# Kernel optimization log

Measured on AMD Instinct MI355X. Metric: run time of the kernel, lower is better.

The kernel has to match this reference:

```python
import jax, jax.numpy as jnp
import numpy as np

F, LP, NL, DG = 65536, 8, 8192, 64
D = 32  # path_state_dim == link_state_dim
ITERS = 8
MS = {'flow_traffic': (0.5, 2.0), 'flow_length': (0.5, 2.0), 'flow_loss_packet': (0.1, 5.0),
      'flow_propag_delay': (0.2, 3.0), 'link_capacity': (1.0, 1.0)}


def gru_cell(h, x, w, u, b):
    # Keras GRUCell (reset_after=True); gate order z, r, h
    mx = x @ w + b[0]
    mh = h @ u + b[1]
    xz, xr, xh = jnp.split(mx, 3, axis=-1)
    hz, hr, hh = jnp.split(mh, 3, axis=-1)
    z = jax.nn.sigmoid(xz + hz)
    r = jax.nn.sigmoid(xr + hr)
    c = jnp.tanh(xh + r * hh)
    return z * h + (1.0 - z) * c


def setup_inputs() -> dict:
    key = jax.random.key(0)
    ks = jax.random.split(key, 24)
    g = lambda i, shape: jax.random.normal(ks[i], shape, jnp.float32) * 0.1
    return dict(
        flow_traffic=jax.random.uniform(ks[0], (F, 1), jnp.float32),
        flow_length=jax.random.uniform(ks[1], (F, 1), jnp.float32),
        flow_loss_packet=jax.random.uniform(ks[2], (F, 1), jnp.float32),
        flow_propag_delay=jax.random.uniform(ks[3], (F, 1), jnp.float32),
        flow_packet_size=jax.random.uniform(ks[4], (F, 1), jnp.float32),
        link_capacity=jax.random.uniform(ks[5], (NL, 1), jnp.float32) + 0.5,
        link_to_flow=jax.random.randint(ks[6], (F, LP), 0, NL),
        flow_to_link_flow=jax.random.randint(ks[7], (NL, DG), 0, F),
        flow_to_link_pos=jax.random.randint(ks[8], (NL, DG), 0, LP + 1),
        fe_w1=g(9, (4, D)), fe_b1=jnp.zeros(D), fe_w2=g(10, (D, D)), fe_b2=jnp.zeros(D),
        le_w1=g(11, (2, D)), le_b1=jnp.zeros(D), le_w2=g(12, (D, D)), le_b2=jnp.zeros(D),
        att_w=g(13, (D, D)), att_b=jnp.zeros(D),
        pg_w=g(14, (D, 3 * D)), pg_u=g(15, (D, 3 * D)), pg_b=jnp.zeros((2, 3 * D)),
        lg_w=g(16, (D, 3 * D)), lg_u=g(17, (D, 3 * D)), lg_b=jnp.zeros((2, 3 * D)),
        ro_w1=g(18, (D, D // 2)), ro_b1=jnp.zeros(D // 2),
        ro_w2=g(19, (D // 2, D // 4)), ro_b2=jnp.zeros(D // 4),
        ro_w3=g(20, (D // 4, 1)), ro_b3=jnp.zeros(1),
    )


def reference(flow_traffic, flow_length, flow_loss_packet, flow_propag_delay, flow_packet_size,
              link_capacity, link_to_flow, flow_to_link_flow, flow_to_link_pos,
              fe_w1, fe_b1, fe_w2, fe_b2, le_w1, le_b1, le_w2, le_b2, att_w, att_b,
              pg_w, pg_u, pg_b, lg_w, lg_u, lg_b, ro_w1, ro_b1, ro_w2, ro_b2, ro_w3, ro_b3):
    norm = lambda x, k: (x - MS[k][0]) * MS[k][1]
    # per-link load: mean of traffic of flows crossing it / capacity  -> [NL,1]
    load = jnp.mean(flow_traffic[flow_to_link_flow], axis=1) / link_capacity
    pf = jnp.concatenate([norm(flow_traffic, 'flow_traffic'), norm(flow_length, 'flow_length'),
                          norm(flow_loss_packet, 'flow_loss_packet'),
                          norm(flow_propag_delay, 'flow_propag_delay')], axis=1)
    path_state = jax.nn.selu(jax.nn.selu(pf @ fe_w1 + fe_b1) @ fe_w2 + fe_b2)  # [F,D]
    lf = jnp.concatenate([norm(link_capacity, 'link_capacity'), load], axis=1)
    link_state = jax.nn.selu(jax.nn.selu(lf @ le_w1 + le_b1) @ le_w2 + le_b2)  # [NL,D]

    pss = None
    for _ in range(ITERS):
        link_gather = link_state[link_to_flow]  # [F,LP,D]
        prev = path_state

        def step(h, x):
            h2 = gru_cell(h, x, pg_w, pg_u, pg_b)
            return h2, h2

        path_state, seq = jax.lax.scan(step, prev, jnp.swapaxes(link_gather, 0, 1))
        seq = jnp.swapaxes(seq, 0, 1)  # [F,LP,D]
        pss = jnp.concatenate([prev[:, None, :], seq], axis=1)  # [F,LP+1,D]
        path_gather = pss[flow_to_link_flow, flow_to_link_pos]  # [NL,DG,D]
        attn = jax.nn.leaky_relu(path_gather @ att_w + att_b, negative_slope=0.2)
        score = jax.nn.softmax(attn, axis=-1)  # K.softmax default axis=-1
        agg = jnp.sum(score * path_gather, axis=1)  # [NL,D]
        link_state = gru_cell(link_state, agg, lg_w, lg_u, lg_b)

    h = jax.nn.selu(pss[:, 1:] @ ro_w1 + ro_b1)
    h = jax.nn.selu(h @ ro_w2 + ro_b2)
    occupancy = jax.nn.softplus(h @ ro_w3 + ro_b3)  # [F,LP,1]
    capacity_gather = link_capacity[link_to_flow]  # [F,LP,1]
    delay = jnp.sum(occupancy / capacity_gather, axis=1)  # [F,1]
    return delay + flow_propag_delay
```

## Files before the change

kernel.cpp:

```cpp
#include <hip/hip_runtime.h>
#include <hip/hip_bf16.h>
#include <cstddef>

#define F_    65536
#define LP_   8
#define NL_   8192
#define DG_   64
#define D_    32
#define ITERS_ 8

typedef short bf16x8 __attribute__((ext_vector_type(8)));
typedef float f32x4 __attribute__((ext_vector_type(4)));
typedef unsigned int u32x4 __attribute__((ext_vector_type(4)));

__device__ __forceinline__ float sigmoidf_(float x) { return 1.0f / (1.0f + __expf(-x)); }
__device__ __forceinline__ float tanhf_(float x)    { return 1.0f - 2.0f / (__expf(2.0f * x) + 1.0f); }
__device__ __forceinline__ float seluf_(float x) {
    const float a = 1.6732632423543772f, s = 1.0507009873554805f;
    return x > 0.0f ? s * x : s * a * (__expf(x) - 1.0f);
}
__device__ __forceinline__ float softplusf_(float x) { return x > 20.0f ? x : log1pf(__expf(x)); }

#define REP32(M) M(0)M(1)M(2)M(3)M(4)M(5)M(6)M(7)M(8)M(9)M(10)M(11)M(12)M(13)M(14)M(15) \
                 M(16)M(17)M(18)M(19)M(20)M(21)M(22)M(23)M(24)M(25)M(26)M(27)M(28)M(29)M(30)M(31)

#define BC32(src, i) __int_as_float(__builtin_amdgcn_ds_swizzle(__float_as_int(src), ((i) << 5)))

__device__ __forceinline__ unsigned int cvtpk_bf16(float a, float b) {
    unsigned int r;
    asm("v_cvt_pk_bf16_f32 %0, %1, %2" : "=v"(r) : "v"(a), "v"(b));
    return r;
}

__device__ __forceinline__ void mk_frag(float4 v0, float4 v1, bf16x8& hi, bf16x8& lo) {
    u32x4 uh;
    uh.x = cvtpk_bf16(v0.x, v0.y);
    uh.y = cvtpk_bf16(v0.z, v0.w);
    uh.z = cvtpk_bf16(v1.x, v1.y);
    uh.w = cvtpk_bf16(v1.z, v1.w);
    float r0 = __uint_as_float(uh.x << 16);
    float r1 = __uint_as_float(uh.x & 0xFFFF0000u);
    float r2 = __uint_as_float(uh.y << 16);
    float r3 = __uint_as_float(uh.y & 0xFFFF0000u);
    float r4 = __uint_as_float(uh.z << 16);
    float r5 = __uint_as_float(uh.z & 0xFFFF0000u);
    float r6 = __uint_as_float(uh.w << 16);
    float r7 = __uint_as_float(uh.w & 0xFFFF0000u);
    u32x4 ul;
    ul.x = cvtpk_bf16(v0.x - r0, v0.y - r1);
    ul.y = cvtpk_bf16(v0.z - r2, v0.w - r3);
    ul.z = cvtpk_bf16(v1.x - r4, v1.y - r5);
    ul.w = cvtpk_bf16(v1.z - r6, v1.w - r7);
    hi = __builtin_bit_cast(bf16x8, uh);
    lo = __builtin_bit_cast(bf16x8, ul);
}

__global__ __launch_bounds__(256) void k_init_path(
    const float* __restrict__ tr, const float* __restrict__ len,
    const float* __restrict__ loss, const float* __restrict__ prop,
    const float* __restrict__ fe_w1, const float* __restrict__ fe_b1,
    const float* __restrict__ fe_w2, const float* __restrict__ fe_b2,
    float* __restrict__ pss)
{
    const int j = threadIdx.x & 31;
    const int half = (threadIdx.x >> 5) & 1;
    float w2c[32];
#pragma unroll
    for (int i = 0; i < 32; i++) w2c[i] = fe_w2[i * 32 + j];
    const float w10 = fe_w1[j], w11 = fe_w1[32 + j], w12 = fe_w1[64 + j], w13 = fe_w1[96 + j];
    const float b1 = fe_b1[j], b2 = fe_b2[j];
    const int wave = (blockIdx.x * blockDim.x + threadIdx.x) >> 6;
    const int nw = (gridDim.x * blockDim.x) >> 6;
    for (int fp = wave; fp < F_ / 2; fp += nw) {
        const int f = fp * 2 + half;
        float p0 = (tr[f]   - 0.5f) * 2.0f;
        float p1 = (len[f]  - 0.5f) * 2.0f;
        float p2 = (loss[f] - 0.1f) * 5.0f;
        float p3 = (prop[f] - 0.2f) * 3.0f;
        float h1 = seluf_(fmaf(p0, w10, fmaf(p1, w11, fmaf(p2, w12, fmaf(p3, w13, b1)))));
        float acc = b2;
#define ISTEP(i) { float hv = BC32(h1, i); acc = fmaf(hv, w2c[i], acc); }
        REP32(ISTEP)
#undef ISTEP
        pss[(size_t)f * 288 + 8 * 32 + j] = seluf_(acc);
    }
}

__global__ __launch_bounds__(256) void k_init_link(
    const float* __restrict__ tr, const float* __restrict__ cap, const int* __restrict__ f2lf,
    const float* __restrict__ le_w1, const float* __restrict__ le_b1,
    const float* __restrict__ le_w2, const float* __restrict__ le_b2,
    float* __restrict__ link_state)
{
    const int lane = threadIdx.x & 63;
    const int j = lane & 31;
    float w2c[32];
#pragma unroll
    for (int i = 0; i < 32; i++) w2c[i] = le_w2[i * 32 + j];
    const float w10 = le_w1[j], w11 = le_w1[32 + j];
    const float b1 = le_b1[j], b2 = le_b2[j];
    const int wave = (blockIdx.x * blockDim.x + threadIdx.x) >> 6;
    const int nw = (gridDim.x * blockDim.x) >> 6;
    for (int l = wave; l < NL_; l += nw) {
        int fidx = f2lf[l * 64 + lane];
        float s = tr[fidx];
        s += __shfl_xor(s, 1);  s += __shfl_xor(s, 2);  s += __shfl_xor(s, 4);
        s += __shfl_xor(s, 8);  s += __shfl_xor(s, 16); s += __shfl_xor(s, 32);
        float c = cap[l];
        float load = s * (1.0f / 64.0f) / c;
        float lf0 = (c - 1.0f);
        float h1 = seluf_(fmaf(lf0, w10, fmaf(load, w11, b1)));
        float acc = b2;
#define LSTEP(i) { float hv = BC32(h1, i); acc = fmaf(hv, w2c[i], acc); }
        REP32(LSTEP)
#undef LSTEP
        if (lane < 32) link_state[l * 32 + j] = seluf_(acc);
    }
}

__global__ __launch_bounds__(256) void k_mx_link(
    const float* __restrict__ link_state, const float* __restrict__ pg_w,
    const float* __restrict__ pg_b, float* __restrict__ mx_link)
{
    const int j = threadIdx.x & 31;
    const int half = (threadIdx.x >> 5) & 1;
    float wz[32], wr[32], wh[32];
#pragma unroll
    for (int i = 0; i < 32; i++) {
        wz[i] = pg_w[i * 96 + j];
        wr[i] = pg_w[i * 96 + 32 + j];
        wh[i] = pg_w[i * 96 + 64 + j];
    }
    const float b0z = pg_b[j], b0r = pg_b[32 + j], b0h = pg_b[64 + j];
    const int wave = (blockIdx.x * blockDim.x + threadIdx.x) >> 6;
    const int nw = (gridDim.x * blockDim.x) >> 6;
    for (int lp = wave; lp < NL_ / 2; lp += nw) {
        const int l = lp * 2 + half;
        float ls = link_state[l * 32 + j];
        float az = b0z, ar = b0r, ah = b0h;
#define MSTEP(i) { float lv = BC32(ls, i); az = fmaf(lv, wz[i], az); ar = fmaf(lv, wr[i], ar); ah = fmaf(lv, wh[i], ah); }
        REP32(MSTEP)
#undef MSTEP
        float* mp = mx_link + l * 96;
        mp[j] = az; mp[32 + j] = ar; mp[64 + j] = ah;
    }
}

__global__ __launch_bounds__(256, 3) void k_path(
    const float* __restrict__ mx_link, const float* __restrict__ pg_u,
    const float* __restrict__ pg_b, const int* __restrict__ l2f,
    float* __restrict__ pss)
{
    __shared__ __align__(16) float xlds[4][576];
    const int lane = threadIdx.x & 63;
    const int wid = threadIdx.x >> 6;
    const int jj = lane & 15;
    const int g4 = lane >> 4;
    const int task = (blockIdx.x * blockDim.x + threadIdx.x) >> 6;
    const int fb = task * 16;

    bf16x8 bhi[6], blo[6];
#pragma unroll
    for (int tl = 0; tl < 6; tl++) {
        const float* up = pg_u + (g4 * 8) * 96 + tl * 16 + jj;
        float4 v0 = make_float4(up[0],   up[96],  up[192], up[288]);
        float4 v1 = make_float4(up[384], up[480], up[576], up[672]);
        mk_frag(v0, v1, bhi[tl], blo[tl]);
    }
    float b1v[6];
#pragma unroll
    for (int g = 0; g < 3; g++) {
#pragma unroll
        for (int hf = 0; hf < 2; hf++)
            b1v[g * 2 + hf] = pg_b[96 + g * 32 + hf * 16 + jj];
    }
    float* pbase = pss + (size_t)(fb + jj) * 288;
    float4 v0 = *(const float4*)(pbase + 256 + g4 * 8);
    float4 v1 = *(const float4*)(pbase + 256 + g4 * 8 + 4);
    *(float4*)(pbase + g4 * 8)     = v0;
    *(float4*)(pbase + g4 * 8 + 4) = v1;
    bf16x8 ahi, alo;
    mk_frag(v0, v1, ahi, alo);
    float hC[4][2];
#pragma unroll
    for (int r = 0; r < 4; r++) {
        const float* hp = pss + (size_t)(fb + 4 * g4 + r) * 288 + 256;
        hC[r][0] = hp[jj];
        hC[r][1] = hp[jj + 16];
    }
    float* wl = &xlds[wid][0];

#pragma unroll
    for (int t = 0; t < 8; t++) {
        float mxv[3][4][2];
#pragma unroll
        for (int r = 0; r < 4; r++) {
            int lk = l2f[(fb + 4 * g4 + r) * 8 + t];
            const float* mp = mx_link + lk * 96;
#pragma unroll
            for (int g = 0; g < 3; g++) {
                mxv[g][r][0] = mp[g * 32 + jj];
                mxv[g][r][1] = mp[g * 32 + jj + 16];
            }
        }
        f32x4 acc[6];
#pragma unroll
        for (int tl = 0; tl < 6; tl++) {
            acc[tl] = f32x4{0.0f, 0.0f, 0.0f, 0.0f};
            acc[tl] = __builtin_amdgcn_mfma_f32_16x16x32_bf16(ahi, bhi[tl], acc[tl], 0, 0, 0);
            acc[tl] = __builtin_amdgcn_mfma_f32_16x16x32_bf16(ahi, blo[tl], acc[tl], 0, 0, 0);
            acc[tl] = __builtin_amdgcn_mfma_f32_16x16x32_bf16(alo, bhi[tl], acc[tl], 0, 0, 0);
        }
#pragma unroll
        for (int r = 0; r < 4; r++) {
#pragma unroll
            for (int hf = 0; hf < 2; hf++) {
                float z  = sigmoidf_(mxv[0][r][hf] + acc[0 + hf][r] + b1v[0 + hf]);
                float rg = sigmoidf_(mxv[1][r][hf] + acc[2 + hf][r] + b1v[2 + hf]);
                float c  = tanhf_(mxv[2][r][hf] + rg * (acc[4 + hf][r] + b1v[4 + hf]));
                float hn = fmaf(z, hC[r][hf], (1.0f - z) * c);
                hC[r][hf] = hn;
                wl[(4 * g4 + r) * 36 + jj + hf * 16] = hn;
            }
        }
        float4 n0 = *(const float4*)&wl[jj * 36 + g4 * 8];
        float4 n1 = *(const float4*)&wl[jj * 36 + g4 * 8 + 4];
        *(float4*)(pbase + (t + 1) * 32 + g4 * 8)     = n0;
        *(float4*)(pbase + (t + 1) * 32 + g4 * 8 + 4) = n1;
        if (t < 7) mk_frag(n0, n1, ahi, alo);
    }
}

__global__ __launch_bounds__(256) void k_att_fused(
    const float* __restrict__ pss, const int* __restrict__ f2lf, const int* __restrict__ f2lp,
    const float* __restrict__ att_w, const float* __restrict__ att_b,
    const float* __restrict__ lg_w, const float* __restrict__ lg_u, const float* __restrict__ lg_b,
    const float* __restrict__ pg_w, const float* __restrict__ pg_b,
    float* __restrict__ link_state, float* __restrict__ mx_link)
{
    __shared__ float red[4][64][33];
    const int w = threadIdx.x >> 6;
    const int lane = threadIdx.x & 63;
    const int l = blockIdx.x * 4 + w;
    const int fi = f2lf[l * 64 + lane];
    const int pi = f2lp[l * 64 + lane];
    const float* row = pss + ((size_t)fi * 9 + pi) * 32;
    float pg[32];
#pragma unroll
    for (int i = 0; i < 8; i++) {
        float4 v = ((const float4*)row)[i];
        pg[4 * i] = v.x; pg[4 * i + 1] = v.y; pg[4 * i + 2] = v.z; pg[4 * i + 3] = v.w;
    }
    float a[32];
#pragma unroll
    for (int jj = 0; jj < 32; jj++) {
        float acc = att_b[jj];
#pragma unroll
        for (int i = 0; i < 32; i++) acc = fmaf(pg[i], att_w[i * 32 + jj], acc);
        a[jj] = acc > 0.0f ? acc : 0.2f * acc;
    }
    float m = a[0];
#pragma unroll
    for (int jj = 1; jj < 32; jj++) m = fmaxf(m, a[jj]);
    float ssum = 0.0f;
#pragma unroll
    for (int jj = 0; jj < 32; jj++) { a[jj] = __expf(a[jj] - m); ssum += a[jj]; }
    float inv = 1.0f / ssum;
    float* myrow = &red[w][lane][0];
#pragma unroll
    for (int jj = 0; jj < 32; jj++) myrow[jj] = a[jj] * inv * pg[jj];
    __syncthreads();
    const int j = lane & 31, hh = lane >> 5;
    float s = 0.0f;
#pragma unroll
    for (int d = 0; d < 32; d++) s += red[w][hh * 32 + d][j];
    s += __shfl_xor(s, 32);
    const float hval = link_state[l * 32 + j];
    float src = (lane < 32) ? hval : s;
    const float* wb = (lane < 32) ? lg_u : lg_w;
    float p0 = (lane < 32) ? lg_b[96 + j]      : lg_b[j];
    float p1 = (lane < 32) ? lg_b[96 + 32 + j] : lg_b[32 + j];
    float p2 = (lane < 32) ? lg_b[96 + 64 + j] : lg_b[64 + j];
#define ASTEP(i) { float v = BC32(src, i); \
    p0 = fmaf(v, wb[(i) * 96 + j], p0); \
    p1 = fmaf(v, wb[(i) * 96 + 32 + j], p1); \
    p2 = fmaf(v, wb[(i) * 96 + 64 + j], p2); }
    REP32(ASTEP)
#undef ASTEP
    float q0 = __shfl_xor(p0, 32);
    float q1 = __shfl_xor(p1, 32);
    float q2 = __shfl_xor(p2, 32);
    float hn = 0.0f;
    if (lane < 32) {
        float z = sigmoidf_(q0 + p0);
        float r = sigmoidf_(q1 + p1);
        float c = tanhf_(q2 + r * p2);
        hn = fmaf(z, hval, (1.0f - z) * c);
        link_state[l * 32 + j] = hn;
    }
    float hnb = __shfl(hn, j);
    float m0 = (lane < 32) ? pg_b[j]      : pg_b[64 + j];
    float m1 = (lane < 32) ? pg_b[32 + j] : 0.0f;
    const float* c0 = (lane < 32) ? pg_w + j      : pg_w + 64 + j;
    const float* c1 = (lane < 32) ? pg_w + 32 + j : pg_w + 64 + j;
#define MXS(i) { float v = BC32(hnb, i); \
    m0 = fmaf(v, c0[(i) * 96], m0); \
    m1 = fmaf(v, c1[(i) * 96], m1); }
    REP32(MXS)
#undef MXS
    float* mp = mx_link + l * 96;
    if (lane < 32) { mp[j] = m0; mp[32 + j] = m1; }
    else           { mp[64 + j] = m0; }
}

__global__ __launch_bounds__(256) void k_readout(
    const float* __restrict__ pss, const int* __restrict__ l2f,
    const float* __restrict__ cap, const float* __restrict__ prop,
    const float* __restrict__ ro_w1, const float* __restrict__ b1,
    const float* __restrict__ ro_w2, const float* __restrict__ b2,
    const float* __restrict__ w3, const float* __restrict__ b3,
    float* __restrict__ out)
{
    const int tid = blockIdx.x * blockDim.x + threadIdx.x;
    const int f = tid >> 3, t = tid & 7;
    const float* row = pss + ((size_t)f * 9 + 1 + t) * 32;
    float xr[32];
#pragma unroll
    for (int i = 0; i < 8; i++) {
        float4 v = ((const float4*)row)[i];
        xr[4 * i] = v.x; xr[4 * i + 1] = v.y; xr[4 * i + 2] = v.z; xr[4 * i + 3] = v.w;
    }
    float h1[16];
#pragma unroll
    for (int jj = 0; jj < 16; jj++) {
        float acc = b1[jj];
#pragma unroll
        for (int i = 0; i < 32; i++) acc = fmaf(xr[i], ro_w1[i * 16 + jj], acc);
        h1[jj] = seluf_(acc);
    }
    float h2[8];
#pragma unroll
    for (int jj = 0; jj < 8; jj++) {
        float acc = b2[jj];
#pragma unroll
        for (int i = 0; i < 16; i++) acc = fmaf(h1[i], ro_w2[i * 8 + jj], acc);
        h2[jj] = seluf_(acc);
    }
    float o = b3[0];
#pragma unroll
    for (int i = 0; i < 8; i++) o = fmaf(h2[i], w3[i], o);
    o = softplusf_(o);
    int link = l2f[f * 8 + t];
    float v = o / cap[link];
    v += __shfl_xor(v, 1, 8);
    v += __shfl_xor(v, 2, 8);
    v += __shfl_xor(v, 4, 8);
    if (t == 0) out[f] = v + prop[f];
}

extern "C" void kernel_launch(void* const* d_in, const int* in_sizes, int n_in,
                              void* d_out, int out_size, void* d_ws, size_t ws_size,
                              hipStream_t stream) {
    const float* flow_traffic = (const float*)d_in[0];
    const float* flow_length  = (const float*)d_in[1];
    const float* flow_loss    = (const float*)d_in[2];
    const float* flow_prop    = (const float*)d_in[3];
    const float* link_cap     = (const float*)d_in[5];
    const int*   l2f          = (const int*)d_in[6];
    const int*   f2lf         = (const int*)d_in[7];
    const int*   f2lp         = (const int*)d_in[8];
    const float* fe_w1 = (const float*)d_in[9],  *fe_b1 = (const float*)d_in[10];
    const float* fe_w2 = (const float*)d_in[11], *fe_b2 = (const float*)d_in[12];
    const float* le_w1 = (const float*)d_in[13], *le_b1 = (const float*)d_in[14];
    const float* le_w2 = (const float*)d_in[15], *le_b2 = (const float*)d_in[16];
    const float* att_w = (const float*)d_in[17], *att_b = (const float*)d_in[18];
    const float* pg_w  = (const float*)d_in[19], *pg_u  = (const float*)d_in[20], *pg_b = (const float*)d_in[21];
    const float* lg_w  = (const float*)d_in[22], *lg_u  = (const float*)d_in[23], *lg_b = (const float*)d_in[24];
    const float* ro_w1 = (const float*)d_in[25], *ro_b1 = (const float*)d_in[26];
    const float* ro_w2 = (const float*)d_in[27], *ro_b2 = (const float*)d_in[28];
    const float* ro_w3 = (const float*)d_in[29], *ro_b3 = (const float*)d_in[30];
    float* out = (float*)d_out;

    float* ws = (float*)d_ws;
    float* pss        = ws;
    float* link_state = pss + (size_t)F_ * 288;
    float* mx_link    = link_state + NL_ * 32;

    k_init_path<<<512, 256, 0, stream>>>(flow_traffic, flow_length, flow_loss, flow_prop,
                                         fe_w1, fe_b1, fe_w2, fe_b2, pss);
    k_init_link<<<512, 256, 0, stream>>>(flow_traffic, link_cap, f2lf,
                                         le_w1, le_b1, le_w2, le_b2, link_state);
    k_mx_link<<<64, 256, 0, stream>>>(link_state, pg_w, pg_b, mx_link);
    for (int it = 0; it < ITERS_; ++it) {
        k_path<<<F_ / 64, 256, 0, stream>>>(mx_link, pg_u, pg_b, l2f, pss);
        k_att_fused<<<NL_ / 4, 256, 0, stream>>>(pss, f2lf, f2lp, att_w, att_b,
                                                 lg_w, lg_u, lg_b, pg_w, pg_b,
                                                 link_state, mx_link);
    }
    k_readout<<<F_ * 8 / 256, 256, 0, stream>>>(pss, l2f, link_cap, flow_prop,
                                                ro_w1, ro_b1, ro_w2, ro_b2, ro_w3, ro_b3, out);
}
```

Before: 652.4 us.

## Use MFMA for attention projection and prefetch next-step link gates in path GRU

The attention kernel's per-lane 32x32 scalar FMA projection is replaced with split-bf16 (hi/lo) 32x32x16 MFMA calls over path rows staged in LDS. Softmax is done across the MFMA output layout, and the weighted sum uses cross-lane shuffle reductions into a small shared buffer. Separately, the path GRU kernel software-prefetches the next timestep's link indices and gathered mx_link values to hide gather latency. These changes aim to cut scalar ALU work and expose memory latency overlap, at the cost of more registers and a change in launch bounds.

```diff
diff --git a/kernel.cpp b/kernel.cpp
--- a/kernel.cpp
+++ b/kernel.cpp
@@ -11,6 +11,7 @@
 
 typedef short bf16x8 __attribute__((ext_vector_type(8)));
 typedef float f32x4 __attribute__((ext_vector_type(4)));
+typedef float f32x16 __attribute__((ext_vector_type(16)));
 typedef unsigned int u32x4 __attribute__((ext_vector_type(4)));
 
 __device__ __forceinline__ float sigmoidf_(float x) { return 1.0f / (1.0f + __expf(-x)); }
@@ -158,6 +159,7 @@
     const int g4 = lane >> 4;
     const int task = (blockIdx.x * blockDim.x + threadIdx.x) >> 6;
     const int fb = task * 16;
+    const int frow = fb + 4 * g4;
 
     bf16x8 bhi[6], blo[6];
 #pragma unroll
@@ -190,17 +192,44 @@
     }
     float* wl = &xlds[wid][0];
 
+    int lk1[4];
+    float mxn[3][4][2];
+#pragma unroll
+    for (int r = 0; r < 4; r++) {
+        int lk0 = l2f[(frow + r) * 8 + 0];
+        const float* mp = mx_link + lk0 * 96;
+#pragma unroll
+        for (int g = 0; g < 3; g++) {
+            mxn[g][r][0] = mp[g * 32 + jj];
+            mxn[g][r][1] = mp[g * 32 + jj + 16];
+        }
+    }
+#pragma unroll
+    for (int r = 0; r < 4; r++) lk1[r] = l2f[(frow + r) * 8 + 1];
+
 #pragma unroll
     for (int t = 0; t < 8; t++) {
         float mxv[3][4][2];
 #pragma unroll
-        for (int r = 0; r < 4; r++) {
-            int lk = l2f[(fb + 4 * g4 + r) * 8 + t];
-            const float* mp = mx_link + lk * 96;
-#pragma unroll
-            for (int g = 0; g < 3; g++) {
-                mxv[g][r][0] = mp[g * 32 + jj];
-                mxv[g][r][1] = mp[g * 32 + jj + 16];
+        for (int g = 0; g < 3; g++)
+#pragma unroll
+            for (int r = 0; r < 4; r++) {
+                mxv[g][r][0] = mxn[g][r][0];
+                mxv[g][r][1] = mxn[g][r][1];
+            }
+        if (t < 7) {
+#pragma unroll
+            for (int r = 0; r < 4; r++) {
+                const float* mp = mx_link + lk1[r] * 96;
+#pragma unroll
+                for (int g = 0; g < 3; g++) {
+                    mxn[g][r][0] = mp[g * 32 + jj];
+                    mxn[g][r][1] = mp[g * 32 + jj + 16];
+                }
+            }
+            if (t < 6) {
+#pragma unroll
+                for (int r = 0; r < 4; r++) lk1[r] = l2f[(frow + r) * 8 + t + 2];
             }
         }
         f32x4 acc[6];
@@ -231,70 +260,130 @@
     }
 }
 
-__global__ __launch_bounds__(256) void k_att_fused(
+__global__ __launch_bounds__(256, 2) void k_att_fused(
     const float* __restrict__ pss, const int* __restrict__ f2lf, const int* __restrict__ f2lp,
     const float* __restrict__ att_w, const float* __restrict__ att_b,
     const float* __restrict__ lg_w, const float* __restrict__ lg_u, const float* __restrict__ lg_b,
     const float* __restrict__ pg_w, const float* __restrict__ pg_b,
     float* __restrict__ link_state, float* __restrict__ mx_link)
 {
-    __shared__ float red[4][64][33];
+    __shared__ float S4[4][64 * 33];
+    __shared__ float xbuf[4][32];
     const int w = threadIdx.x >> 6;
     const int lane = threadIdx.x & 63;
+    const int p31 = lane & 31;
+    const int h = lane >> 5;
     const int l = blockIdx.x * 4 + w;
+    const int j = p31;
+    float* S = &S4[w][0];
+
     const int fi = f2lf[l * 64 + lane];
     const int pi = f2lp[l * 64 + lane];
     const float* row = pss + ((size_t)fi * 9 + pi) * 32;
-    float pg[32];
 #pragma unroll
     for (int i = 0; i < 8; i++) {
         float4 v = ((const float4*)row)[i];
-        pg[4 * i] = v.x; pg[4 * i + 1] = v.y; pg[4 * i + 2] = v.z; pg[4 * i + 3] = v.w;
-    }
-    float a[32];
-#pragma unroll
-    for (int jj = 0; jj < 32; jj++) {
-        float acc = att_b[jj];
-#pragma unroll
-        for (int i = 0; i < 32; i++) acc = fmaf(pg[i], att_w[i * 32 + jj], acc);
-        a[jj] = acc > 0.0f ? acc : 0.2f * acc;
-    }
-    float m = a[0];
-#pragma unroll
-    for (int jj = 1; jj < 32; jj++) m = fmaxf(m, a[jj]);
-    float ssum = 0.0f;
-#pragma unroll
-    for (int jj = 0; jj < 32; jj++) { a[jj] = __expf(a[jj] - m); ssum += a[jj]; }
-    float inv = 1.0f / ssum;
-    float* myrow = &red[w][lane][0];
-#pragma unroll
-    for (int jj = 0; jj < 32; jj++) myrow[jj] = a[jj] * inv * pg[jj];
-    __syncthreads();
-    const int j = lane & 31, hh = lane >> 5;
-    float s = 0.0f;
-#pragma unroll
-    for (int d = 0; d < 32; d++) s += red[w][hh * 32 + d][j];
-    s += __shfl_xor(s, 32);
+        S[lane * 33 + 4 * i + 0] = v.x;
+        S[lane * 33 + 4 * i + 1] = v.y;
+        S[lane * 33 + 4 * i + 2] = v.z;
+        S[lane * 33 + 4 * i + 3] = v.w;
+    }
+
+    bf16x8 awhi[2], awlo[2];
+#pragma unroll
+    for (int kt = 0; kt < 2; kt++) {
+        const float* wp = att_w + (kt * 16 + h * 8) * 32 + p31;
+        float4 a0 = make_float4(wp[0],   wp[32],  wp[64],  wp[96]);
+        float4 a1 = make_float4(wp[128], wp[160], wp[192], wp[224]);
+        mk_frag(a0, a1, awhi[kt], awlo[kt]);
+    }
+    float4 ab[4];
+#pragma unroll
+    for (int rg = 0; rg < 4; rg++) ab[rg] = *(const float4*)(att_b + 8 * rg + 4 * h);
+
+    bf16x8 bphi[2][2], bplo[2][2];
+#pragma unroll
+    for (int ph = 0; ph < 2; ph++)
+#pragma unroll
+        for (int kt = 0; kt < 2; kt++) {
+            const float* sp = S + (p31 + 32 * ph) * 33 + kt * 16 + h * 8;
+            float4 b0 = make_float4(sp[0], sp[1], sp[2], sp[3]);
+            float4 b1 = make_float4(sp[4], sp[5], sp[6], sp[7]);
+            mk_frag(b0, b1, bphi[ph][kt], bplo[ph][kt]);
+        }
+
+    f32x16 acc0{}, acc1{};
+#pragma unroll
+    for (int kt = 0; kt < 2; kt++) {
+        acc0 = __builtin_amdgcn_mfma_f32_32x32x16_bf16(awhi[kt], bphi[0][kt], acc0, 0, 0, 0);
+        acc0 = __builtin_amdgcn_mfma_f32_32x32x16_bf16(awhi[kt], bplo[0][kt], acc0, 0, 0, 0);
+        acc0 = __builtin_amdgcn_mfma_f32_32x32x16_bf16(awlo[kt], bphi[0][kt], acc0, 0, 0, 0);
+        acc1 = __builtin_amdgcn_mfma_f32_32x32x16_bf16(awhi[kt], bphi[1][kt], acc1, 0, 0, 0);
+        acc1 = __builtin_amdgcn_mfma_f32_32x32x16_bf16(awhi[kt], bplo[1][kt], acc1, 0, 0, 0);
+        acc1 = __builtin_amdgcn_mfma_f32_32x32x16_bf16(awlo[kt], bphi[1][kt], acc1, 0, 0, 0);
+    }
+
+    float q0[16], q1[16];
+#pragma unroll
+    for (int ph = 0; ph < 2; ph++) {
+        float v[16];
+#pragma unroll
+        for (int r = 0; r < 16; r++) {
+            float bias = ((const float*)&ab[r >> 2])[r & 3];
+            float x = (ph == 0 ? acc0[r] : acc1[r]) + bias;
+            v[r] = x > 0.0f ? x : 0.2f * x;
+        }
+        float m = v[0];
+#pragma unroll
+        for (int r = 1; r < 16; r++) m = fmaxf(m, v[r]);
+        m = fmaxf(m, __shfl_xor(m, 32));
+        float sm = 0.0f;
+#pragma unroll
+        for (int r = 0; r < 16; r++) { v[r] = __expf(v[r] - m); sm += v[r]; }
+        sm += __shfl_xor(sm, 32);
+        float inv = 1.0f / sm;
+        const float* sp = S + (p31 + 32 * ph) * 33;
+        float* q = (ph == 0) ? q0 : q1;
+#pragma unroll
+        for (int r = 0; r < 16; r++) {
+            int jr = (r & 3) + 8 * (r >> 2) + 4 * h;
+            q[r] = v[r] * inv * sp[jr];
+        }
+    }
+    float qs[16];
+#pragma unroll
+    for (int r = 0; r < 16; r++) qs[r] = q0[r] + q1[r];
+#pragma unroll
+    for (int d = 1; d < 32; d <<= 1) {
+#pragma unroll
+        for (int r = 0; r < 16; r++) qs[r] += __shfl_xor(qs[r], d);
+    }
+    if (p31 == 0) {
+#pragma unroll
+        for (int r = 0; r < 16; r++) xbuf[w][(r & 3) + 8 * (r >> 2) + 4 * h] = qs[r];
+    }
+    float s = xbuf[w][j];
+
     const float hval = link_state[l * 32 + j];
     float src = (lane < 32) ? hval : s;
     const float* wb = (lane < 32) ? lg_u : lg_w;
     float p0 = (lane < 32) ? lg_b[96 + j]      : lg_b[j];
     float p1 = (lane < 32) ? lg_b[96 + 32 + j] : lg_b[32 + j];
     float p2 = (lane < 32) ? lg_b[96 + 64 + j] : lg_b[64 + j];
-#define ASTEP(i) { float v = BC32(src, i); \
-    p0 = fmaf(v, wb[(i) * 96 + j], p0); \
-    p1 = fmaf(v, wb[(i) * 96 + 32 + j], p1); \
-    p2 = fmaf(v, wb[(i) * 96 + 64 + j], p2); }
+#define ASTEP(i) { float vv = BC32(src, i); \
+    p0 = fmaf(vv, wb[(i) * 96 + j], p0); \
+    p1 = fmaf(vv, wb[(i) * 96 + 32 + j], p1); \
+    p2 = fmaf(vv, wb[(i) * 96 + 64 + j], p2); }
     REP32(ASTEP)
 #undef ASTEP
-    float q0 = __shfl_xor(p0, 32);
-    float q1 = __shfl_xor(p1, 32);
-    float q2 = __shfl_xor(p2, 32);
+    float t0 = __shfl_xor(p0, 32);
+    float t1 = __shfl_xor(p1, 32);
+    float t2 = __shfl_xor(p2, 32);
     float hn = 0.0f;
     if (lane < 32) {
-        float z = sigmoidf_(q0 + p0);
-        float r = sigmoidf_(q1 + p1);
-        float c = tanhf_(q2 + r * p2);
+        float z = sigmoidf_(t0 + p0);
+        float r = sigmoidf_(t1 + p1);
+        float c = tanhf_(t2 + r * p2);
         hn = fmaf(z, hval, (1.0f - z) * c);
         link_state[l * 32 + j] = hn;
     }
@@ -303,9 +392,9 @@
     float m1 = (lane < 32) ? pg_b[32 + j] : 0.0f;
     const float* c0 = (lane < 32) ? pg_w + j      : pg_w + 64 + j;
     const float* c1 = (lane < 32) ? pg_w + 32 + j : pg_w + 64 + j;
-#define MXS(i) { float v = BC32(hnb, i); \
-    m0 = fmaf(v, c0[(i) * 96], m0); \
-    m1 = fmaf(v, c1[(i) * 96], m1); }
+#define MXS(i) { float vv = BC32(hnb, i); \
+    m0 = fmaf(vv, c0[(i) * 96], m0); \
+    m1 = fmaf(vv, c1[(i) * 96], m1); }
     REP32(MXS)
 #undef MXS
     float* mp = mx_link + l * 96;
```

Measured after the change: 655.3 us. Within noise of the previous version (+0.4%).
